# Kernel optimization log

Hardware: AMD Instinct MI355X
Metric: run time of the kernel (lower is better)

## Reference

```python
import jax, jax.numpy as jnp
import numpy as np

B, EMB, HT, WD = 32, 256, 56, 56
NH, WS, SHIFTED = 8, 4, True


def setup_inputs() -> dict:
    key = jax.random.key(0)
    ks = jax.random.split(key, 6)
    x = jax.random.normal(ks[0], (B, EMB, HT, WD), jnp.float32)
    s = 1.0 / np.sqrt(EMB)
    w1 = jax.random.uniform(ks[1], (3 * EMB, EMB), jnp.float32, -s, s)
    b1 = jax.random.uniform(ks[2], (3 * EMB,), jnp.float32, -s, s)
    w2 = jax.random.uniform(ks[3], (EMB, EMB), jnp.float32, -s, s)
    b2 = jax.random.uniform(ks[4], (EMB,), jnp.float32, -s, s)
    pos_emb = jax.random.normal(ks[5], (2 * WS - 1, 2 * WS - 1), jnp.float32)
    return {"x": x, "w1": w1, "b1": b1, "w2": w2, "b2": b2, "pos_emb": pos_emb}


def _rel_indices(ws):
    coords = np.array([[i, j] for i in range(ws) for j in range(ws)])
    rel = coords[None, :, :] - coords[:, None, :] + ws - 1  # (ws^2, ws^2, 2)
    return jnp.asarray(rel)


def _shift_masks(ws):
    m = np.zeros((ws * ws, ws * ws), np.float32)
    s = ws * (ws // 2)
    m[-s:, :-s] = -np.inf
    m[:-s, -s:] = -np.inf
    # '(r w1) (c w2) -> (w1 r) (w2 c)' with r=c=ws
    col = m.reshape(ws, ws, ws, ws).transpose(1, 0, 3, 2).reshape(ws * ws, ws * ws)
    return jnp.asarray(m), jnp.asarray(col)


def reference(x, w1, b1, w2, b2, pos_emb):
    b, c, ht, wd = x.shape
    ws, nh = WS, NH
    e = c // nh
    # b c h w -> b (h w) c, then QKV projection
    xt = x.reshape(b, c, ht * wd).transpose(0, 2, 1)
    qkv = xt @ w1.T + b1                      # (b, hw, 3c)
    # '(c k)' with c outer, k inner -> reshape (..., c, 3)
    qkv = qkv.reshape(b, ht, wd, c, 3)
    if SHIFTED:
        qkv = jnp.roll(qkv, (-ws // 2, -ws // 2), axis=(1, 2))
    Wh, Ww = ht // ws, wd // ws
    # 'b (Wh w1) (Ww w2) (e H) k -> b H Wh Ww (w1 w2) e k'  (e outer, H inner)
    qkv = qkv.reshape(b, Wh, ws, Ww, ws, e, nh, 3)
    qkv = qkv.transpose(0, 6, 1, 3, 2, 4, 5, 7).reshape(b, nh, Wh, Ww, ws * ws, e, 3)
    Q, K, V = qkv[..., 0], qkv[..., 1], qkv[..., 2]
    scale = jnp.sqrt(jnp.float32(c / nh))
    wei = jnp.einsum('bhijpe,bhijqe->bhijpq', Q, K) / scale  # (b,H,Wh,Ww,ws^2,ws^2)
    rel = _rel_indices(ws)
    wei = wei + pos_emb[rel[..., 0], rel[..., 1]]
    if SHIFTED:
        row_mask, col_mask = _shift_masks(ws)
        wei = wei.at[:, :, -1, :].add(row_mask)
        wei = wei.at[:, :, :, -1].add(col_mask)
    attn = jax.nn.softmax(wei, axis=-1)
    out = jnp.einsum('bhijpq,bhijqe->bhijpe', attn, V)
    # 'b H Wh Ww (w1 w2) e -> b (Wh w1) (Ww w2) (H e)'
    out = out.reshape(b, nh, Wh, Ww, ws, ws, e)
    out = out.transpose(0, 2, 4, 3, 5, 1, 6).reshape(b, ht, wd, nh * e)
    out = out.reshape(b, ht * wd, c)
    return out @ w2.T + b2
```

## Files before the change

kernel.cpp:

```cpp
#include <hip/hip_runtime.h>
#include <hip/hip_bf16.h>
#include <math.h>

typedef __attribute__((ext_vector_type(8))) short short8;
typedef __attribute__((ext_vector_type(4))) short short4_;
typedef __attribute__((ext_vector_type(4))) float f32x4;

#define B_    32
#define C_    256
#define HW_   3136
#define N1_   768
#define NWIN_ 14
#define M_    100352

__device__ __forceinline__ short bf16_of(float f) {
  union { __hip_bfloat16 h; short s; } u;
  u.h = __float2bfloat16(f);
  return u.s;
}

__device__ __forceinline__ void load_lds16(const void* g, void* l) {
  __builtin_amdgcn_global_load_lds(
      (const __attribute__((address_space(1))) unsigned int*)g,
      (__attribute__((address_space(3))) unsigned int*)l, 16, 0, 0);
}

__device__ __forceinline__ f32x4 mfma16x16x16bf16(short4_ a, short4_ b, f32x4 c) {
#if __has_builtin(__builtin_amdgcn_mfma_f32_16x16x16bf16_1k)
  return __builtin_amdgcn_mfma_f32_16x16x16bf16_1k(a, b, c, 0, 0, 0);
#else
  asm volatile("v_mfma_f32_16x16x16_bf16 %0, %1, %2, %0\n\ts_nop 7\n\ts_nop 7"
               : "+v"(c) : "v"(a), "v"(b));
  return c;
#endif
}

__global__ void conv_weights(const float* __restrict__ w1, const float* __restrict__ w2,
                             const float* __restrict__ b1,
                             short* __restrict__ w1p, short* __restrict__ w2b,
                             float* __restrict__ b1p) {
  int i = blockIdx.x * 256 + threadIdx.x;
  if (i < 196608) {
    const int r = i >> 8, c = i & 255;
    const int k = r >> 8, rem = r & 255, h = rem >> 5, e = rem & 31;
    const int orig = 24 * e + 3 * h + k;
    w1p[i] = bf16_of(w1[orig * 256 + c]);
  }
  if (i < 65536) w2b[i] = bf16_of(w2[i]);
  if (i < 768) {
    const int k = i >> 8, rem = i & 255, h = rem >> 5, e = rem & 31;
    b1p[i] = b1[24 * e + 3 * h + k];
  }
}

__global__ __launch_bounds__(256) void transpose_x(const float* __restrict__ x,
                                                   short* __restrict__ xt) {
  __shared__ __align__(16) short T[64 * 256];
  const int t = threadIdx.x;
  const int m0 = blockIdx.x * 64;
  const int b  = m0 / HW_;
  const int hw0 = m0 - b * HW_;
  const int tq = (t & 15) * 4;
  const int cg = t >> 4;

#pragma unroll
  for (int p = 0; p < 4; ++p) {
    const int cc = (p * 16 + cg) * 4;
    const float* xp = x + ((size_t)b * C_ + cc) * HW_ + hw0 + tq;
    float4 v0 = *(const float4*)(xp);
    float4 v1 = *(const float4*)(xp + HW_);
    float4 v2 = *(const float4*)(xp + 2 * HW_);
    float4 v3 = *(const float4*)(xp + 3 * HW_);
    const int cq = p * 16 + cg;
#define WR_(i, e0, e1, e2, e3)                                        \
    { const int row = tq + i;                                         \
      short4_ wv; wv[0] = bf16_of(e0); wv[1] = bf16_of(e1);           \
      wv[2] = bf16_of(e2); wv[3] = bf16_of(e3);                       \
      *(short4_*)&T[row * 256 + ((cq ^ ((row >> 2) & 7)) << 2)] = wv; }
    WR_(0, v0.x, v1.x, v2.x, v3.x)
    WR_(1, v0.y, v1.y, v2.y, v3.y)
    WR_(2, v0.z, v1.z, v2.z, v3.z)
    WR_(3, v0.w, v1.w, v2.w, v3.w)
#undef WR_
  }
  __syncthreads();

#pragma unroll
  for (int it = 0; it < 8; ++it) {
    const int idx = it * 256 + t;
    const int row = idx >> 5, ch16 = idx & 31;
    const int s = (row >> 2) & 7;
    const int cqa = (ch16 * 2) ^ s, cqb = (ch16 * 2 + 1) ^ s;
    int2 lo = *(const int2*)&T[row * 256 + cqa * 4];
    int2 hi = *(const int2*)&T[row * 256 + cqb * 4];
    int4 o = make_int4(lo.x, lo.y, hi.x, hi.y);
    *(int4*)(xt + (size_t)(m0 + row) * C_ + ch16 * 8) = o;
  }
}

__global__ __launch_bounds__(256) void qkv_gemm(const short* __restrict__ xt,
    const short* __restrict__ w1p, const float* __restrict__ b1p,
    short* __restrict__ qkvb) {
  __shared__ char smem[32768];
  char* As = smem;
  char* Bs = smem + 16384;
  const int t = threadIdx.x, l = t & 63, w = t >> 6;
  const int d = blockIdx.x, xcd = d & 7, i0 = d >> 3;
  const int bn = i0 % 6, bm = (i0 / 6) * 8 + xcd;
  const int m0 = bm * 128, n0 = bn * 128;
  const int lane = l & 15, kg = l >> 4;
  const int wm = w >> 1, wn = w & 1;

  f32x4 acc[4][4];
#pragma unroll
  for (int i = 0; i < 4; ++i)
#pragma unroll
    for (int j = 0; j < 4; ++j) acc[i][j] = (f32x4){0.f, 0.f, 0.f, 0.f};

  for (int ks = 0; ks < 4; ++ks) {
    const int k0 = ks * 64;
#pragma unroll
    for (int q = 0; q < 4; ++q) {
      const int row = (w * 4 + q) * 8 + (l >> 3);
      const int sc  = (l & 7) ^ (row & 7);
      load_lds16(xt  + (size_t)(m0 + row) * 256 + k0 + sc * 8, As + (w * 4 + q) * 1024);
      load_lds16(w1p + (size_t)(n0 + row) * 256 + k0 + sc * 8, Bs + (w * 4 + q) * 1024);
    }
    __syncthreads();
#pragma unroll
    for (int s = 0; s < 2; ++s) {
      short8 a[4], b[4];
#pragma unroll
      for (int i = 0; i < 4; ++i) {
        const int r = wm * 64 + i * 16 + lane;
        a[i] = *(const short8*)(As + r * 128 + ((s * 64 + kg * 16) ^ ((r & 7) << 4)));
      }
#pragma unroll
      for (int j = 0; j < 4; ++j) {
        const int r = wn * 64 + j * 16 + lane;
        b[j] = *(const short8*)(Bs + r * 128 + ((s * 64 + kg * 16) ^ ((r & 7) << 4)));
      }
#pragma unroll
      for (int i = 0; i < 4; ++i)
#pragma unroll
        for (int j = 0; j < 4; ++j)
          acc[i][j] = __builtin_amdgcn_mfma_f32_16x16x32_bf16(a[i], b[j], acc[i][j], 0, 0, 0);
    }
    __syncthreads();
  }

#pragma unroll
  for (int j = 0; j < 4; ++j) {
    const int n = n0 + wn * 64 + j * 16 + lane;
    const float bias = b1p[n];
#pragma unroll
    for (int i = 0; i < 4; ++i) {
      const int mb = m0 + wm * 64 + i * 16 + kg * 4;
#pragma unroll
      for (int r = 0; r < 4; ++r)
        qkvb[(size_t)(mb + r) * N1_ + n] = bf16_of(acc[i][j][r] + bias);
    }
  }
}

__global__ __launch_bounds__(512) void win_attn(const short* __restrict__ qkvb,
    const float* __restrict__ pos, short* __restrict__ attnb) {
  __shared__ __align__(16) short Sq[16 * 768];
  __shared__ __align__(16) short Ot[16 * 272];
  __shared__ float Pe[49];

  const int t = threadIdx.x, l = t & 63, h = t >> 6;
  if (t < 49) Pe[t] = pos[t];

  const int win = blockIdx.x;
  const int wxi = win % NWIN_;
  const int wyi = (win / NWIN_) % NWIN_;
  const int b   = win / (NWIN_ * NWIN_);

#pragma unroll
  for (int rep = 0; rep < 3; ++rep) {
    const int idx = rep * 512 + t;
    const int row = idx / 96, ch = idx % 96;
    const int pr = row >> 2, pc = row & 3;
    int y  = wyi * 4 + pr + 2; if (y >= 56) y -= 56;
    int xx = wxi * 4 + pc + 2; if (xx >= 56) xx -= 56;
    const size_t m = (size_t)b * HW_ + y * 56 + xx;
    int4 v = *(const int4*)(qkvb + m * N1_ + ch * 8);
    *(int4*)(Sq + row * 768 + (ch ^ (row & 7)) * 8) = v;
  }
  __syncthreads();

  const int lane = l & 15, kg = l >> 4;

  const int cQ = h * 4 + kg;
  short8 qf = *(const short8*)(Sq + lane * 768 + ((cQ)      ^ (lane & 7)) * 8);
  short8 kf = *(const short8*)(Sq + lane * 768 + ((32 + cQ) ^ (lane & 7)) * 8);

  f32x4 z = {0.f, 0.f, 0.f, 0.f};
  f32x4 st = __builtin_amdgcn_mfma_f32_16x16x32_bf16(kf, qf, z, 0, 0, 0);

  const int pr = lane >> 2, pc = lane & 3;
  const float rscale = 0.17677669529663687f;
  float sv[4];
#pragma unroll
  for (int r = 0; r < 4; ++r) {
    const int q = kg * 4 + r, qr = q >> 2, qc = q & 3;
    float s = st[r] * rscale + Pe[(qr - pr + 3) * 7 + (qc - pc + 3)];
    if (wyi == NWIN_ - 1 && ((pr >= 2) != (qr >= 2))) s = -1e30f;
    if (wxi == NWIN_ - 1 && ((pc >= 2) != (qc >= 2))) s = -1e30f;
    sv[r] = s;
  }
  float mx = fmaxf(fmaxf(sv[0], sv[1]), fmaxf(sv[2], sv[3]));
  mx = fmaxf(mx, __shfl_xor(mx, 16));
  mx = fmaxf(mx, __shfl_xor(mx, 32));
  float ex[4], sm = 0.f;
#pragma unroll
  for (int r = 0; r < 4; ++r) { ex[r] = __expf(sv[r] - mx); sm += ex[r]; }
  sm += __shfl_xor(sm, 16);
  sm += __shfl_xor(sm, 32);
  const float inv = 1.0f / sm;
  short4_ pf;
#pragma unroll
  for (int r = 0; r < 4; ++r) pf[r] = bf16_of(ex[r] * inv);

#pragma unroll
  for (int half = 0; half < 2; ++half) {
    short4_ vf;
    const int cV = 64 + h * 4 + half * 2 + (lane >> 3);
    const int el = lane & 7;
#pragma unroll
    for (int i = 0; i < 4; ++i) {
      const int vrow = kg * 4 + i;
      vf[i] = Sq[vrow * 768 + (cV ^ (vrow & 7)) * 8 + el];
    }
    f32x4 o = mfma16x16x16bf16(pf, vf, z);
#pragma unroll
    for (int r = 0; r < 4; ++r)
      Ot[(kg * 4 + r) * 272 + h * 32 + half * 16 + lane] = bf16_of(o[r]);
  }
  __syncthreads();

  const int row = t >> 5, ch = t & 31;
  const short* rp = &Ot[row * 272 + ch * 8];
  int4 v = *(const int4*)rp;
  const size_t mo = (size_t)b * HW_ + (wyi * 4 + (row >> 2)) * 56 + wxi * 4 + (row & 3);
  *(int4*)(attnb + mo * C_ + ch * 8) = v;
}

__global__ __launch_bounds__(256) void proj_gemm(const short* __restrict__ attnb,
    const short* __restrict__ w2b, const float* __restrict__ b2,
    float* __restrict__ out) {
  __shared__ char smem[32768];
  char* As = smem;
  char* Bs = smem + 16384;
  const int t = threadIdx.x, l = t & 63, w = t >> 6;
  const int d = blockIdx.x, xcd = d & 7, i0 = d >> 3;
  const int bn = i0 & 1, bm = (i0 >> 1) * 8 + xcd;
  const int m0 = bm * 128, n0 = bn * 128;
  const int lane = l & 15, kg = l >> 4;
  const int wm = w >> 1, wn = w & 1;

  f32x4 acc[4][4];
#pragma unroll
  for (int i = 0; i < 4; ++i)
#pragma unroll
    for (int j = 0; j < 4; ++j) acc[i][j] = (f32x4){0.f, 0.f, 0.f, 0.f};

  for (int ks = 0; ks < 4; ++ks) {
    const int k0 = ks * 64;
#pragma unroll
    for (int q = 0; q < 4; ++q) {
      const int row = (w * 4 + q) * 8 + (l >> 3);
      const int sc  = (l & 7) ^ (row & 7);
      load_lds16(attnb + (size_t)(m0 + row) * 256 + k0 + sc * 8, As + (w * 4 + q) * 1024);
      load_lds16(w2b   + (size_t)(n0 + row) * 256 + k0 + sc * 8, Bs + (w * 4 + q) * 1024);
    }
    __syncthreads();
#pragma unroll
    for (int s = 0; s < 2; ++s) {
      short8 a[4], b[4];
#pragma unroll
      for (int i = 0; i < 4; ++i) {
        const int r = wm * 64 + i * 16 + lane;
        a[i] = *(const short8*)(As + r * 128 + ((s * 64 + kg * 16) ^ ((r & 7) << 4)));
      }
#pragma unroll
      for (int j = 0; j < 4; ++j) {
        const int r = wn * 64 + j * 16 + lane;
        b[j] = *(const short8*)(Bs + r * 128 + ((s * 64 + kg * 16) ^ ((r & 7) << 4)));
      }
#pragma unroll
      for (int i = 0; i < 4; ++i)
#pragma unroll
        for (int j = 0; j < 4; ++j)
          acc[i][j] = __builtin_amdgcn_mfma_f32_16x16x32_bf16(a[i], b[j], acc[i][j], 0, 0, 0);
    }
    __syncthreads();
  }

#pragma unroll
  for (int j = 0; j < 4; ++j) {
    const int n = n0 + wn * 64 + j * 16 + lane;
    const float bias = b2[n];
#pragma unroll
    for (int i = 0; i < 4; ++i) {
      const int mb = m0 + wm * 64 + i * 16 + kg * 4;
#pragma unroll
      for (int r = 0; r < 4; ++r)
        out[(size_t)(mb + r) * C_ + n] = acc[i][j][r] + bias;
    }
  }
}

extern "C" void kernel_launch(void* const* d_in, const int* in_sizes, int n_in,
                              void* d_out, int out_size, void* d_ws, size_t ws_size,
                              hipStream_t stream) {
  const float* x   = (const float*)d_in[0];
  const float* w1  = (const float*)d_in[1];
  const float* b1  = (const float*)d_in[2];
  const float* w2  = (const float*)d_in[3];
  const float* b2  = (const float*)d_in[4];
  const float* pos = (const float*)d_in[5];
  float* out = (float*)d_out;

  char* ws = (char*)d_ws;
  short* xt    = (short*)ws;
  short* qkvb  = (short*)(ws + (size_t)52000000);
  short* attnb = (short*)(ws + (size_t)52000000 + 155000000);
  short* w1p   = (short*)(ws + (size_t)52000000 + 155000000 + 52000000);
  short* w2b   = w1p + 196608;
  float* b1p   = (float*)(w2b + 65536);

  conv_weights<<<768, 256, 0, stream>>>(w1, w2, b1, w1p, w2b, b1p);
  transpose_x <<<1568, 256, 0, stream>>>(x, xt);
  qkv_gemm    <<<4704, 256, 0, stream>>>(xt, w1p, b1p, qkvb);
  win_attn    <<<6272, 512, 0, stream>>>(qkvb, pos, attnb);
  proj_gemm   <<<1568, 256, 0, stream>>>(attnb, w2b, b2, out);
}
```

Measured before the change: 349.8 us.

## Fuse input transpose into QKV GEMM and output projection into window attention

The QKV GEMM now reads the fp32 NCHW input directly, converting to bf16 and transposing into swizzled LDS, which removes the separate transpose kernel and its intermediate buffer. The output projection is moved into the window-attention kernel: each block multiplies its 16x256 attention tile by w2 with MFMA, reading w2 straight from global memory, and writes the fp32 output. This drops two launches and the round trips of the xt and attnb intermediates. In exchange, x is reloaded by each of the six N-tiles of the QKV GEMM with less coalesced strided loads, and every attention block re-reads all of w2 from cache without LDS staging.

```diff
diff --git a/kernel.cpp b/kernel.cpp
--- a/kernel.cpp
+++ b/kernel.cpp
@@ -53,52 +53,7 @@
   }
 }
 
-__global__ __launch_bounds__(256) void transpose_x(const float* __restrict__ x,
-                                                   short* __restrict__ xt) {
-  __shared__ __align__(16) short T[64 * 256];
-  const int t = threadIdx.x;
-  const int m0 = blockIdx.x * 64;
-  const int b  = m0 / HW_;
-  const int hw0 = m0 - b * HW_;
-  const int tq = (t & 15) * 4;
-  const int cg = t >> 4;
-
-#pragma unroll
-  for (int p = 0; p < 4; ++p) {
-    const int cc = (p * 16 + cg) * 4;
-    const float* xp = x + ((size_t)b * C_ + cc) * HW_ + hw0 + tq;
-    float4 v0 = *(const float4*)(xp);
-    float4 v1 = *(const float4*)(xp + HW_);
-    float4 v2 = *(const float4*)(xp + 2 * HW_);
-    float4 v3 = *(const float4*)(xp + 3 * HW_);
-    const int cq = p * 16 + cg;
-#define WR_(i, e0, e1, e2, e3)                                        \
-    { const int row = tq + i;                                         \
-      short4_ wv; wv[0] = bf16_of(e0); wv[1] = bf16_of(e1);           \
-      wv[2] = bf16_of(e2); wv[3] = bf16_of(e3);                       \
-      *(short4_*)&T[row * 256 + ((cq ^ ((row >> 2) & 7)) << 2)] = wv; }
-    WR_(0, v0.x, v1.x, v2.x, v3.x)
-    WR_(1, v0.y, v1.y, v2.y, v3.y)
-    WR_(2, v0.z, v1.z, v2.z, v3.z)
-    WR_(3, v0.w, v1.w, v2.w, v3.w)
-#undef WR_
-  }
-  __syncthreads();
-
-#pragma unroll
-  for (int it = 0; it < 8; ++it) {
-    const int idx = it * 256 + t;
-    const int row = idx >> 5, ch16 = idx & 31;
-    const int s = (row >> 2) & 7;
-    const int cqa = (ch16 * 2) ^ s, cqb = (ch16 * 2 + 1) ^ s;
-    int2 lo = *(const int2*)&T[row * 256 + cqa * 4];
-    int2 hi = *(const int2*)&T[row * 256 + cqb * 4];
-    int4 o = make_int4(lo.x, lo.y, hi.x, hi.y);
-    *(int4*)(xt + (size_t)(m0 + row) * C_ + ch16 * 8) = o;
-  }
-}
-
-__global__ __launch_bounds__(256) void qkv_gemm(const short* __restrict__ xt,
+__global__ __launch_bounds__(256) void qkv_gemm(const float* __restrict__ x,
     const short* __restrict__ w1p, const float* __restrict__ b1p,
     short* __restrict__ qkvb) {
   __shared__ char smem[32768];
@@ -123,8 +78,32 @@
     for (int q = 0; q < 4; ++q) {
       const int row = (w * 4 + q) * 8 + (l >> 3);
       const int sc  = (l & 7) ^ (row & 7);
-      load_lds16(xt  + (size_t)(m0 + row) * 256 + k0 + sc * 8, As + (w * 4 + q) * 1024);
       load_lds16(w1p + (size_t)(n0 + row) * 256 + k0 + sc * 8, Bs + (w * 4 + q) * 1024);
+    }
+#pragma unroll
+    for (int it = 0; it < 2; ++it) {
+      const int qid = it * 256 + t;
+      const int tm4 = qid & 31;
+      const int tk4 = qid >> 5;
+      const int m4g = m0 + tm4 * 4;
+      const int bb = m4g / HW_;
+      const int hw = m4g - bb * HW_;
+      const float* xp = x + ((size_t)bb * C_ + k0 + tk4 * 4) * HW_ + hw;
+      float4 v0 = *(const float4*)(xp);
+      float4 v1 = *(const float4*)(xp + HW_);
+      float4 v2 = *(const float4*)(xp + 2 * HW_);
+      float4 v3 = *(const float4*)(xp + 3 * HW_);
+      const int c16 = tk4 >> 1, lo8 = (tk4 & 1) * 8;
+#define WRA_(i2, e0, e1, e2, e3)                                       \
+      { const int r = tm4 * 4 + i2;                                    \
+        short4_ wv; wv[0] = bf16_of(e0); wv[1] = bf16_of(e1);          \
+        wv[2] = bf16_of(e2); wv[3] = bf16_of(e3);                      \
+        *(short4_*)(As + r * 128 + ((c16 ^ (r & 7)) << 4) + lo8) = wv; }
+      WRA_(0, v0.x, v1.x, v2.x, v3.x)
+      WRA_(1, v0.y, v1.y, v2.y, v3.y)
+      WRA_(2, v0.z, v1.z, v2.z, v3.z)
+      WRA_(3, v0.w, v1.w, v2.w, v3.w)
+#undef WRA_
     }
     __syncthreads();
 #pragma unroll
@@ -164,7 +143,8 @@
 }
 
 __global__ __launch_bounds__(512) void win_attn(const short* __restrict__ qkvb,
-    const float* __restrict__ pos, short* __restrict__ attnb) {
+    const float* __restrict__ pos, const short* __restrict__ w2b,
+    const float* __restrict__ b2, float* __restrict__ out) {
   __shared__ __align__(16) short Sq[16 * 768];
   __shared__ __align__(16) short Ot[16 * 272];
   __shared__ float Pe[49];
@@ -240,75 +220,25 @@
   }
   __syncthreads();
 
-  const int row = t >> 5, ch = t & 31;
-  const short* rp = &Ot[row * 272 + ch * 8];
-  int4 v = *(const int4*)rp;
-  const size_t mo = (size_t)b * HW_ + (wyi * 4 + (row >> 2)) * 56 + wxi * 4 + (row & 3);
-  *(int4*)(attnb + mo * C_ + ch * 8) = v;
-}
-
-__global__ __launch_bounds__(256) void proj_gemm(const short* __restrict__ attnb,
-    const short* __restrict__ w2b, const float* __restrict__ b2,
-    float* __restrict__ out) {
-  __shared__ char smem[32768];
-  char* As = smem;
-  char* Bs = smem + 16384;
-  const int t = threadIdx.x, l = t & 63, w = t >> 6;
-  const int d = blockIdx.x, xcd = d & 7, i0 = d >> 3;
-  const int bn = i0 & 1, bm = (i0 >> 1) * 8 + xcd;
-  const int m0 = bm * 128, n0 = bn * 128;
-  const int lane = l & 15, kg = l >> 4;
-  const int wm = w >> 1, wn = w & 1;
-
-  f32x4 acc[4][4];
-#pragma unroll
-  for (int i = 0; i < 4; ++i)
-#pragma unroll
-    for (int j = 0; j < 4; ++j) acc[i][j] = (f32x4){0.f, 0.f, 0.f, 0.f};
-
-  for (int ks = 0; ks < 4; ++ks) {
-    const int k0 = ks * 64;
-#pragma unroll
-    for (int q = 0; q < 4; ++q) {
-      const int row = (w * 4 + q) * 8 + (l >> 3);
-      const int sc  = (l & 7) ^ (row & 7);
-      load_lds16(attnb + (size_t)(m0 + row) * 256 + k0 + sc * 8, As + (w * 4 + q) * 1024);
-      load_lds16(w2b   + (size_t)(n0 + row) * 256 + k0 + sc * 8, Bs + (w * 4 + q) * 1024);
-    }
-    __syncthreads();
-#pragma unroll
-    for (int s = 0; s < 2; ++s) {
-      short8 a[4], b[4];
-#pragma unroll
-      for (int i = 0; i < 4; ++i) {
-        const int r = wm * 64 + i * 16 + lane;
-        a[i] = *(const short8*)(As + r * 128 + ((s * 64 + kg * 16) ^ ((r & 7) << 4)));
-      }
-#pragma unroll
-      for (int j = 0; j < 4; ++j) {
-        const int r = wn * 64 + j * 16 + lane;
-        b[j] = *(const short8*)(Bs + r * 128 + ((s * 64 + kg * 16) ^ ((r & 7) << 4)));
-      }
-#pragma unroll
-      for (int i = 0; i < 4; ++i)
-#pragma unroll
-        for (int j = 0; j < 4; ++j)
-          acc[i][j] = __builtin_amdgcn_mfma_f32_16x16x32_bf16(a[i], b[j], acc[i][j], 0, 0, 0);
-    }
-    __syncthreads();
-  }
-
-#pragma unroll
-  for (int j = 0; j < 4; ++j) {
-    const int n = n0 + wn * 64 + j * 16 + lane;
-    const float bias = b2[n];
-#pragma unroll
-    for (int i = 0; i < 4; ++i) {
-      const int mb = m0 + wm * 64 + i * 16 + kg * 4;
-#pragma unroll
-      for (int r = 0; r < 4; ++r)
-        out[(size_t)(mb + r) * C_ + n] = acc[i][j][r] + bias;
-    }
+  f32x4 pacc0 = z, pacc1 = z;
+  const int n0p = h * 32;
+#pragma unroll
+  for (int ksp = 0; ksp < 8; ++ksp) {
+    const int koff = ksp * 32 + kg * 8;
+    short8 af  = *(const short8*)(Ot + lane * 272 + koff);
+    short8 bf0 = *(const short8*)(w2b + (size_t)(n0p + lane) * 256 + koff);
+    short8 bf1 = *(const short8*)(w2b + (size_t)(n0p + 16 + lane) * 256 + koff);
+    pacc0 = __builtin_amdgcn_mfma_f32_16x16x32_bf16(af, bf0, pacc0, 0, 0, 0);
+    pacc1 = __builtin_amdgcn_mfma_f32_16x16x32_bf16(af, bf1, pacc1, 0, 0, 0);
+  }
+  const int ncol = n0p + lane;
+  const float bias0 = b2[ncol], bias1 = b2[ncol + 16];
+#pragma unroll
+  for (int r = 0; r < 4; ++r) {
+    const int m = kg * 4 + r;
+    const size_t mo = (size_t)b * HW_ + (wyi * 4 + (m >> 2)) * 56 + wxi * 4 + (m & 3);
+    out[mo * C_ + ncol]      = pacc0[r] + bias0;
+    out[mo * C_ + ncol + 16] = pacc1[r] + bias1;
   }
 }
 
@@ -324,16 +254,12 @@
   float* out = (float*)d_out;
 
   char* ws = (char*)d_ws;
-  short* xt    = (short*)ws;
-  short* qkvb  = (short*)(ws + (size_t)52000000);
-  short* attnb = (short*)(ws + (size_t)52000000 + 155000000);
-  short* w1p   = (short*)(ws + (size_t)52000000 + 155000000 + 52000000);
-  short* w2b   = w1p + 196608;
-  float* b1p   = (float*)(w2b + 65536);
+  short* qkvb = (short*)ws;
+  short* w1p  = (short*)(ws + (size_t)155000000);
+  short* w2b  = w1p + 196608;
+  float* b1p  = (float*)(w2b + 65536);
 
   conv_weights<<<768, 256, 0, stream>>>(w1, w2, b1, w1p, w2b, b1p);
-  transpose_x <<<1568, 256, 0, stream>>>(x, xt);
-  qkv_gemm    <<<4704, 256, 0, stream>>>(xt, w1p, b1p, qkvb);
-  win_attn    <<<6272, 512, 0, stream>>>(qkvb, pos, attnb);
-  proj_gemm   <<<1568, 256, 0, stream>>>(attnb, w2b, b2, out);
-}
+  qkv_gemm    <<<4704, 256, 0, stream>>>(x, w1p, b1p, qkvb);
+  win_attn    <<<6272, 512, 0, stream>>>(qkvb, pos, w2b, b2, out);
+}
```

Result: slower. 375.1 us (+7.2%).
